# Optimization experiments

Hardware: AMD Instinct MI355X
Metric: run time of the kernel (lower is better)

## Reference

```python
import jax, jax.numpy as jnp
import numpy as np

B, IN_UNITS, IN_CH, NUM_UNITS, UNIT_SIZE = 32, 16, 2048, 16, 64
NUM_ITERS = 2


def setup_inputs() -> dict:
    key = jax.random.key(0)
    k1, k2 = jax.random.split(key)
    x = jax.random.normal(k1, (B, IN_UNITS, IN_CH), dtype=jnp.float32)
    W = jax.random.normal(k2, (1, IN_CH, NUM_UNITS, UNIT_SIZE, IN_UNITS), dtype=jnp.float32)
    return {"x": x, "W": W}


def squash(s):
    # torch code sums squared magnitude over dim=2 (the num_units axis) with keepdim
    mag_sq = jnp.sum(s * s, axis=2, keepdims=True)
    mag = jnp.sqrt(mag_sq)
    return mag_sq / (1.0 + mag_sq) * (s / mag)


def reference(x, W):
    # x: (B, in_units, in_channels) -> (B, in_channels, in_units)
    xt = jnp.swapaxes(x, 1, 2)
    # u_hat[b,i,j,k] = sum_u W[0,i,j,k,u] * xt[b,i,u]  -> (B, IC, NU, US)
    u_hat = jnp.einsum('ijku,biu->bijk', W[0], xt)
    b_ij = jnp.zeros((1, IN_CH, NUM_UNITS, 1), dtype=x.dtype)
    v_j = None
    for _ in range(NUM_ITERS):
        # softmax over a singleton trailing dim -> all ones (faithful to source)
        c_ij = jax.nn.softmax(b_ij, axis=-1)  # (1, IC, NU, 1), broadcasts over batch
        s_j = jnp.sum(c_ij[None, ..., 0][0][None].squeeze(0) * 0 + c_ij * u_hat, axis=1, keepdims=True) if False else jnp.sum(c_ij * u_hat, axis=1, keepdims=True)  # (B,1,NU,US)
        v_j = squash(s_j)  # (B,1,NU,US)
        # agreement: <u_hat, v_j> over unit_size, broadcast v_j over in_channels
        u_vj1 = jnp.einsum('bijk,bljk->bij', u_hat, v_j)  # (B, IC, NU)
        u_vj1 = jnp.mean(u_vj1, axis=0, keepdims=True)[..., None]  # (1, IC, NU, 1)
        b_ij = b_ij + u_vj1
    return v_j[:, 0, :, :]  # (B, num_units, unit_size)
```

## Files before the change

### kernel.cpp

```cpp
#include <hip/hip_runtime.h>
#include <hip/hip_bf16.h>


#define B_SZ   32
#define IC     2048
#define NJ     16
#define NK     64
#define SOUT   (B_SZ*NJ*NK)
#define KSTEPS 1024
#define KSPLIT 32
#define SPW    (KSTEPS/KSPLIT)

typedef float v4f __attribute__((ext_vector_type(4)));
typedef short v8s __attribute__((ext_vector_type(8)));

static __device__ inline ushort f2bf(float f) {
    uint32_t u = __float_as_uint(f);
    u += 0x7FFFu + ((u >> 16) & 1u);
    return (ushort)(u >> 16);
}

__global__ __launch_bounds__(256)
void caps_main(const float* __restrict__ x, const float* __restrict__ W,
               float* __restrict__ part) {
    __shared__ ushort axb[SPW * 1024];
    const int tid   = threadIdx.x;
    const int j     = blockIdx.x;
    const int split = blockIdx.y;
    const int i0    = split * 64;

    #pragma unroll
    for (int it = 0; it < 8; ++it) {
        int w = it * 256 + tid;
        int r = w >> 2;
        int c = w & 3;
        int b = r >> 4;
        int u = r & 15;
        const float* xp = x + (size_t)b * 32768 + (size_t)u * 2048 + i0 + c * 16;
        v4f f0 = *(const v4f*)(xp);
        v4f f1 = *(const v4f*)(xp + 4);
        v4f f2 = *(const v4f*)(xp + 8);
        v4f f3 = *(const v4f*)(xp + 12);
        float ff[16] = {f0.x, f0.y, f0.z, f0.w, f1.x, f1.y, f1.z, f1.w,
                        f2.x, f2.y, f2.z, f2.w, f3.x, f3.y, f3.z, f3.w};
        const int mtoff = (b >> 4) * 512;
        const int bl    = b & 15;
        const int qlo   = u >> 3;
        const int jj    = u & 7;
        #pragma unroll
        for (int e = 0; e < 16; ++e) {
            int il   = c * 16 + e;
            int q    = qlo | ((il & 1) << 1);
            int addr = (il >> 1) * 1024 + mtoff + ((bl | (q << 4)) * 8) + jj;
            axb[addr] = f2bf(ff[e]);
        }
    }
    __syncthreads();

    const int wv   = tid >> 6;
    const int lane = tid & 63;
    const int n    = lane & 15;
    const int q    = lane >> 4;
    const int step0 = split * SPW;

    v4f acc0 = {0.f, 0.f, 0.f, 0.f};
    v4f acc1 = {0.f, 0.f, 0.f, 0.f};

    const float* wp = W + (size_t)(2 * step0 + (q >> 1)) * 16384
                        + (size_t)j * 1024 + (size_t)(wv * 16 + n) * 16 + (q & 1) * 8;
    const ushort* xl = axb + lane * 8;

    #pragma unroll 4
    for (int s = 0; s < SPW; ++s) {
        v4f w0 = *(const v4f*)(wp);
        v4f w1 = *(const v4f*)(wp + 4);
        v8s a0 = *(const v8s*)(xl);
        v8s a1 = *(const v8s*)(xl + 512);
        v8s bb;
        bb[0] = (short)f2bf(w0.x); bb[1] = (short)f2bf(w0.y);
        bb[2] = (short)f2bf(w0.z); bb[3] = (short)f2bf(w0.w);
        bb[4] = (short)f2bf(w1.x); bb[5] = (short)f2bf(w1.y);
        bb[6] = (short)f2bf(w1.z); bb[7] = (short)f2bf(w1.w);
        acc0 = __builtin_amdgcn_mfma_f32_16x16x32_bf16(a0, bb, acc0, 0, 0, 0);
        acc1 = __builtin_amdgcn_mfma_f32_16x16x32_bf16(a1, bb, acc1, 0, 0, 0);
        wp += 2 * 16384;
        xl += 1024;
    }

    float* pp = part + (size_t)split * SOUT + (size_t)j * NK + wv * 16 + n;
    #pragma unroll
    for (int r = 0; r < 4; ++r) {
        int m = q * 4 + r;
        pp[(size_t)m * 1024]        = acc0[r];
        pp[(size_t)(m + 16) * 1024] = acc1[r];
    }
}

__global__ __launch_bounds__(256)
void caps_finish(const float* __restrict__ part, float* __restrict__ out) {
    __shared__ float ls[256];
    __shared__ float l2[64];
    const int bid = blockIdx.x;
    const int b   = bid >> 4;
    const int k0  = (bid & 15) * 4;
    const int tid = threadIdx.x;
    const int jj  = tid >> 4;
    const int kc  = (tid >> 2) & 3;
    const int sg  = tid & 3;
    const size_t idx = (size_t)b * 1024 + (size_t)jj * NK + k0 + kc;

    float s = 0.0f;
    #pragma unroll
    for (int ss = 0; ss < KSPLIT / 4; ++ss)
        s += part[(size_t)(sg + 4 * ss) * SOUT + idx];
    ls[tid] = s;
    __syncthreads();

    if (sg == 0)
        l2[jj * 4 + kc] = ls[tid] + ls[tid + 1] + ls[tid + 2] + ls[tid + 3];
    __syncthreads();

    if (sg == 0) {
        float sa  = l2[jj * 4 + kc];
        float msq = 0.0f;
        #pragma unroll
        for (int j2 = 0; j2 < NJ; ++j2) {
            float v = l2[j2 * 4 + kc];
            msq += v * v;
        }
        float mag = sqrtf(msq);
        out[idx] = sa * (mag / (1.0f + msq));
    }
}

extern "C" void kernel_launch(void* const* d_in, const int* in_sizes, int n_in,
                              void* d_out, int out_size, void* d_ws, size_t ws_size,
                              hipStream_t stream) {
    const float* x = (const float*)d_in[0];
    const float* W = (const float*)d_in[1];
    float* out  = (float*)d_out;

    float* part = (float*)d_ws;

    caps_main  <<<dim3(NJ, KSPLIT), 256, 0, stream>>>(x, W, part);
    caps_finish<<<512,              256, 0, stream>>>(part, out);
}
```

Before: 207.7 us.

## Split x bf16 conversion into a prep kernel and use packed bf16 conversion

New measurement: 201.6 us. 2.9% less time.

```diff
diff --git a/kernel.cpp b/kernel.cpp
--- a/kernel.cpp
+++ b/kernel.cpp
@@ -11,80 +11,95 @@
 #define KSPLIT 32
 #define SPW    (KSTEPS/KSPLIT)
 
-typedef float v4f __attribute__((ext_vector_type(4)));
-typedef short v8s __attribute__((ext_vector_type(8)));
+typedef float  v4f __attribute__((ext_vector_type(4)));
+typedef short  v8s __attribute__((ext_vector_type(8)));
+typedef uint   v4u __attribute__((ext_vector_type(4)));
 
-static __device__ inline ushort f2bf(float f) {
-    uint32_t u = __float_as_uint(f);
-    u += 0x7FFFu + ((u >> 16) & 1u);
-    return (ushort)(u >> 16);
+static __device__ inline uint pk2(float a, float b) {
+    __hip_bfloat162 h = __float22bfloat162_rn(make_float2(a, b));
+    uint r;
+    __builtin_memcpy(&r, &h, 4);
+    return r;
 }
 
 __global__ __launch_bounds__(256)
-void caps_main(const float* __restrict__ x, const float* __restrict__ W,
-               float* __restrict__ part) {
-    __shared__ ushort axb[SPW * 1024];
-    const int tid   = threadIdx.x;
-    const int j     = blockIdx.x;
-    const int split = blockIdx.y;
-    const int i0    = split * 64;
+void caps_xprep(const float* __restrict__ x, ushort* __restrict__ xb) {
+    __shared__ ushort tile[256 * 18];
+    const int t  = threadIdx.x;
+    const int i0 = blockIdx.x * 16;
+    const int mt = blockIdx.y;
 
-    #pragma unroll
-    for (int it = 0; it < 8; ++it) {
-        int w = it * 256 + tid;
-        int r = w >> 2;
-        int c = w & 3;
-        int b = r >> 4;
-        int u = r & 15;
-        const float* xp = x + (size_t)b * 32768 + (size_t)u * 2048 + i0 + c * 16;
+    {
+        const int r2 = t;
+        const float* xp = x + (size_t)(mt * 256 + r2) * IC + i0;
         v4f f0 = *(const v4f*)(xp);
         v4f f1 = *(const v4f*)(xp + 4);
         v4f f2 = *(const v4f*)(xp + 8);
         v4f f3 = *(const v4f*)(xp + 12);
-        float ff[16] = {f0.x, f0.y, f0.z, f0.w, f1.x, f1.y, f1.z, f1.w,
-                        f2.x, f2.y, f2.z, f2.w, f3.x, f3.y, f3.z, f3.w};
-        const int mtoff = (b >> 4) * 512;
-        const int bl    = b & 15;
-        const int qlo   = u >> 3;
-        const int jj    = u & 7;
+        uint d[8] = {pk2(f0.x, f0.y), pk2(f0.z, f0.w), pk2(f1.x, f1.y), pk2(f1.z, f1.w),
+                     pk2(f2.x, f2.y), pk2(f2.z, f2.w), pk2(f3.x, f3.y), pk2(f3.z, f3.w)};
+        const int swz = ((r2 >> 3) & 7) << 1;
         #pragma unroll
-        for (int e = 0; e < 16; ++e) {
-            int il   = c * 16 + e;
-            int q    = qlo | ((il & 1) << 1);
-            int addr = (il >> 1) * 1024 + mtoff + ((bl | (q << 4)) * 8) + jj;
-            axb[addr] = f2bf(ff[e]);
-        }
+        for (int c = 0; c < 8; ++c)
+            *(uint*)&tile[r2 * 18 + ((2 * c) ^ swz)] = d[c];
     }
     __syncthreads();
 
-    const int wv   = tid >> 6;
-    const int lane = tid & 63;
-    const int n    = lane & 15;
-    const int q    = lane >> 4;
+    #pragma unroll
+    for (int rr = 0; rr < 2; ++rr) {
+        const int idx   = rr * 256 + t;
+        const int stepl = idx >> 6;
+        const int lane  = idx & 63;
+        const int q  = lane >> 4;
+        const int bl = lane & 15;
+        const int il = 2 * stepl + (q >> 1);
+        const int rb = bl * 16 + (q & 1) * 8;
+        const int swz = ((rb >> 3) & 7) << 1;
+        ushort v[8];
+        #pragma unroll
+        for (int jj = 0; jj < 8; ++jj)
+            v[jj] = tile[(rb + jj) * 18 + (il ^ swz)];
+        const int stepg = blockIdx.x * 8 + stepl;
+        *(v8s*)(xb + (size_t)stepg * 1024 + mt * 512 + lane * 8) = *(const v8s*)v;
+    }
+}
+
+__global__ __launch_bounds__(256)
+void caps_mfma(const ushort* __restrict__ xb, const float* __restrict__ W,
+               float* __restrict__ part) {
+    const int tid   = threadIdx.x;
+    const int wv    = tid >> 6;
+    const int lane  = tid & 63;
+    const int j     = blockIdx.x;
+    const int split = blockIdx.y;
+    const int n     = lane & 15;
+    const int q     = lane >> 4;
     const int step0 = split * SPW;
 
     v4f acc0 = {0.f, 0.f, 0.f, 0.f};
     v4f acc1 = {0.f, 0.f, 0.f, 0.f};
 
-    const float* wp = W + (size_t)(2 * step0 + (q >> 1)) * 16384
-                        + (size_t)j * 1024 + (size_t)(wv * 16 + n) * 16 + (q & 1) * 8;
-    const ushort* xl = axb + lane * 8;
+    const float*  wp = W + (size_t)(2 * step0 + (q >> 1)) * 16384
+                         + (size_t)j * 1024 + (size_t)(wv * 16 + n) * 16 + (q & 1) * 8;
+    const ushort* xp = xb + (size_t)step0 * 1024 + (size_t)lane * 8;
 
     #pragma unroll 4
     for (int s = 0; s < SPW; ++s) {
         v4f w0 = *(const v4f*)(wp);
         v4f w1 = *(const v4f*)(wp + 4);
-        v8s a0 = *(const v8s*)(xl);
-        v8s a1 = *(const v8s*)(xl + 512);
+        v8s a0 = *(const v8s*)(xp);
+        v8s a1 = *(const v8s*)(xp + 512);
+        v4u bu;
+        bu[0] = pk2(w0.x, w0.y);
+        bu[1] = pk2(w0.z, w0.w);
+        bu[2] = pk2(w1.x, w1.y);
+        bu[3] = pk2(w1.z, w1.w);
         v8s bb;
-        bb[0] = (short)f2bf(w0.x); bb[1] = (short)f2bf(w0.y);
-        bb[2] = (short)f2bf(w0.z); bb[3] = (short)f2bf(w0.w);
-        bb[4] = (short)f2bf(w1.x); bb[5] = (short)f2bf(w1.y);
-        bb[6] = (short)f2bf(w1.z); bb[7] = (short)f2bf(w1.w);
+        __builtin_memcpy(&bb, &bu, 16);
         acc0 = __builtin_amdgcn_mfma_f32_16x16x32_bf16(a0, bb, acc0, 0, 0, 0);
         acc1 = __builtin_amdgcn_mfma_f32_16x16x32_bf16(a1, bb, acc1, 0, 0, 0);
         wp += 2 * 16384;
-        xl += 1024;
+        xp += 1024;
     }
 
     float* pp = part + (size_t)split * SOUT + (size_t)j * NK + wv * 16 + n;
@@ -140,8 +155,10 @@
     const float* W = (const float*)d_in[1];
     float* out  = (float*)d_out;
 
-    float* part = (float*)d_ws;
+    float*  part = (float*)d_ws;
+    ushort* xb   = (ushort*)(part + (size_t)KSPLIT * SOUT);
 
-    caps_main  <<<dim3(NJ, KSPLIT), 256, 0, stream>>>(x, W, part);
+    caps_xprep <<<dim3(128, 2),     256, 0, stream>>>(x, xb);
+    caps_mfma  <<<dim3(NJ, KSPLIT), 256, 0, stream>>>(xb, W, part);
     caps_finish<<<512,              256, 0, stream>>>(part, out);
 }
```
